# Kernel optimization log

Hardware: AMD Instinct MI355X
Metric: run time of the kernel (lower is better)

Reference implementation:

```python
import jax, jax.numpy as jnp
import numpy as np

N, IN_DIM, OUT_DIM, H = 4096, 128, 128, 4
HEAD_DIM = OUT_DIM // H
NEG_SLOPE = 0.2


def setup_inputs() -> dict:
    key = jax.random.key(0)
    k1, k2, k3, k4, k5 = jax.random.split(key, 5)
    x = jax.random.normal(k1, (N, IN_DIM), dtype=jnp.float32)
    adj = jax.random.randint(k2, (N, N), 0, 2, dtype=jnp.int32)
    # nn.Linear(in_dim, out_dim, bias=False): weight is [out_dim, in_dim]
    W = jax.random.normal(k3, (OUT_DIM, IN_DIM), dtype=jnp.float32) * (1.0 / np.sqrt(IN_DIM))
    attn_src = jax.random.normal(k4, (1, H, HEAD_DIM), dtype=jnp.float32) * 0.1
    attn_dst = jax.random.normal(k5, (1, H, HEAD_DIM), dtype=jnp.float32) * 0.1
    return {"x": x, "adj": adj, "W": W, "attn_src": attn_src, "attn_dst": attn_dst}


def reference(x, adj, W, attn_src, attn_dst):
    n = x.shape[0]
    h = (x @ W.T).reshape(n, H, HEAD_DIM)            # [N, H, D]
    e_src = jnp.sum(h * attn_src, axis=-1)           # [N, H]
    e_dst = jnp.sum(h * attn_dst, axis=-1)           # [N, H]
    e = e_src[:, None, :] + e_dst[None, :, :]        # [N, N, H]
    e = jax.nn.leaky_relu(e, negative_slope=NEG_SLOPE)
    e = jnp.where((adj == 0)[:, :, None], -jnp.inf, e)
    alpha = jax.nn.softmax(e, axis=1)                # softmax over neighbors j
    # dropout omitted (eval mode)
    out = jnp.einsum('ijh,jhd->ihd', alpha, h)       # [N, H, D]
    return out.reshape(n, -1)
```

## Files before the change

### kernel.cpp

```cpp
#include <hip/hip_runtime.h>
#include <hip/hip_bf16.h>

#define NN 4096
#define SJ 8
#define JCH (NN / SJ)
#define JSTEP 64
#define NSTEPS (JCH / JSTEP)
#define ROWS 16
#define LOG2E 1.44269504f

typedef __attribute__((ext_vector_type(4))) float f32x4;
typedef __attribute__((ext_vector_type(4))) int i32x4;
typedef __attribute__((ext_vector_type(4))) unsigned int u32x4;
typedef __attribute__((ext_vector_type(8))) short short8;

__device__ __forceinline__ unsigned pk2(float a, float b) {
    float2 t; t.x = a; t.y = b;
    __hip_bfloat162 h = __float22bfloat162_rn(t);
    unsigned r;
    __builtin_memcpy(&r, &h, 4);
    return r;
}

__device__ __forceinline__ short8 load8_bf(const float* __restrict__ p) {
    f32x4 a = *(const f32x4*)p;
    f32x4 b = *(const f32x4*)(p + 4);
    u32x4 v = {pk2(a[0], a[1]), pk2(a[2], a[3]), pk2(b[0], b[1]), pk2(b[2], b[3])};
    return __builtin_bit_cast(short8, v);
}

__global__ __launch_bounds__(256) void k1_proj(
        const float* __restrict__ x, const float* __restrict__ W,
        const float* __restrict__ asrc, const float* __restrict__ adst,
        unsigned short* __restrict__ hT, float* __restrict__ Rt,
        unsigned* __restrict__ BDt) {
    __shared__ unsigned short ttile[4][32][16];
    const int ibase = blockIdx.x * 16;
    const int w = threadIdx.x >> 6;
    const int lane = threadIdx.x & 63;
    const int grp = lane >> 4, li = lane & 15;

    const float* xrow = x + (ibase + li) * 128;
    const float* w0 = W + (w * 32 + li) * 128;
    const float* w1 = W + (w * 32 + 16 + li) * 128;

    f32x4 c0 = {0.f, 0.f, 0.f, 0.f}, c1 = {0.f, 0.f, 0.f, 0.f};
#pragma unroll
    for (int ko = 0; ko < 128; ko += 32) {
        const int kk = ko + grp * 8;
        short8 a = load8_bf(xrow + kk);
        short8 b0 = load8_bf(w0 + kk);
        short8 b1 = load8_bf(w1 + kk);
        c0 = __builtin_amdgcn_mfma_f32_16x16x32_bf16(a, b0, c0, 0, 0, 0);
        c1 = __builtin_amdgcn_mfma_f32_16x16x32_bf16(a, b1, c1, 0, 0, 0);
    }
    const float as0 = asrc[w * 32 + li], as1 = asrc[w * 32 + 16 + li];
    const float ad0 = adst[w * 32 + li], ad1 = adst[w * 32 + 16 + li];
    float pes[4], ped[4];
#pragma unroll
    for (int r = 0; r < 4; ++r) {
        pes[r] = c0[r] * as0 + c1[r] * as1;
        ped[r] = c0[r] * ad0 + c1[r] * ad1;
    }
#pragma unroll
    for (int m = 1; m < 16; m <<= 1) {
#pragma unroll
        for (int r = 0; r < 4; ++r) {
            pes[r] += __shfl_xor(pes[r], m);
            ped[r] += __shfl_xor(ped[r], m);
        }
    }
    if (li == 0) {
#pragma unroll
        for (int r = 0; r < 4; ++r) {
            const int row = ibase + grp * 4 + r;
            Rt[w * NN + row] = __builtin_amdgcn_exp2f(-0.8f * LOG2E * pes[r]);
            const float Bv = __builtin_amdgcn_exp2f(LOG2E * ped[r]);
            const float Dv = __builtin_amdgcn_exp2f(0.2f * LOG2E * ped[r]);
            BDt[w * NN + row] = pk2(Bv, Dv);
        }
    }
    unsigned short* tw = &ttile[w][0][0];
    {
        uint2 v0; v0.x = pk2(c0[0], c0[1]); v0.y = pk2(c0[2], c0[3]);
        uint2 v1; v1.x = pk2(c1[0], c1[1]); v1.y = pk2(c1[2], c1[3]);
        *(uint2*)&tw[li * 16 + grp * 4] = v0;
        *(uint2*)&tw[(li + 16) * 16 + grp * 4] = v1;
    }
    __syncthreads();
    const int d = lane >> 1, half = lane & 1;
    u32x4 v = *(const u32x4*)&ttile[w][d][half * 8];
    *(u32x4*)(hT + (size_t)(w * 32 + d) * NN + ibase + half * 8) = v;
}

struct SR {
    short8 t00, t01, t10, t11;
    u32x4 b0a, b0b, b1a, b1b;
};

__device__ __forceinline__ short8 buildQ(float R, const u32x4 ba, const u32x4 bb,
                                         const i32x4 q0, const i32x4 q1) {
    float p[8];
#pragma unroll
    for (int e = 0; e < 4; ++e) {
        const unsigned v = ba[e];
        const float B = __builtin_bit_cast(float, v << 16);
        const float D = __builtin_bit_cast(float, v & 0xFFFF0000u);
        const float m = fmaxf(B, R * D);
        p[e] = __builtin_bit_cast(float, __builtin_bit_cast(unsigned, m) & (0u - (unsigned)q0[e]));
    }
#pragma unroll
    for (int e = 0; e < 4; ++e) {
        const unsigned v = bb[e];
        const float B = __builtin_bit_cast(float, v << 16);
        const float D = __builtin_bit_cast(float, v & 0xFFFF0000u);
        const float m = fmaxf(B, R * D);
        p[4 + e] = __builtin_bit_cast(float, __builtin_bit_cast(unsigned, m) & (0u - (unsigned)q1[e]));
    }
    u32x4 u = {pk2(p[0], p[1]), pk2(p[2], p[3]), pk2(p[4], p[5]), pk2(p[6], p[7])};
    return __builtin_bit_cast(short8, u);
}

__global__ __launch_bounds__(256, 4) void k3_main(
        const int* __restrict__ adj, const unsigned short* __restrict__ hT,
        const float* __restrict__ Rt, const unsigned* __restrict__ BDt,
        float* __restrict__ numer, float* __restrict__ denom) {
    __shared__ unsigned int adjbuf[3][ROWS * 64];

    const int ibase = blockIdx.x * ROWS;
    const int jstart = blockIdx.y * JCH;
    const int head = threadIdx.x >> 6;
    const int lane = threadIdx.x & 63;
    const int grp = lane >> 4, li = lane & 15;

    const float Rv = Rt[head * NN + ibase + li];
    const unsigned short* h0 = hT + (size_t)(head * 32 + li) * NN + jstart;
    const unsigned short* h1 = hT + (size_t)(head * 32 + 16 + li) * NN + jstart;
    const unsigned* bd = BDt + head * NN + jstart;
    const unsigned int* adju = (const unsigned int*)adj;

    const int srow = head * 4 + grp;
    const unsigned int* gsrc = adju + (size_t)(ibase + srow) * NN + jstart + (li ^ srow) * 4;

    f32x4 c0 = {0.f,0.f,0.f,0.f}, c1 = {0.f,0.f,0.f,0.f}, dn = {0.f,0.f,0.f,0.f};
    short8 bones;
#pragma unroll
    for (int e = 0; e < 8; ++e) bones[e] = (short)0x3F80;

    auto stage = [&](int slot, int toff) {
        __builtin_amdgcn_global_load_lds(gsrc + toff, &adjbuf[slot][head * 4 * 64], 16, 0, 0);
    };
    auto loadR = [&](int toff) {
        SR r;
        r.t00 = *(const short8*)(h0 + toff + grp * 8);
        r.t01 = *(const short8*)(h0 + toff + 32 + grp * 8);
        r.t10 = *(const short8*)(h1 + toff + grp * 8);
        r.t11 = *(const short8*)(h1 + toff + 32 + grp * 8);
        r.b0a = *(const u32x4*)(bd + toff + grp * 8);
        r.b0b = *(const u32x4*)(bd + toff + grp * 8 + 4);
        r.b1a = *(const u32x4*)(bd + toff + 32 + grp * 8);
        r.b1b = *(const u32x4*)(bd + toff + 32 + grp * 8 + 4);
        return r;
    };
    auto compute = [&](const unsigned int* buf, const SR& S) {
#pragma unroll
        for (int ks = 0; ks < 2; ++ks) {
            const short8 tA = ks ? S.t01 : S.t00;
            const short8 tB = ks ? S.t11 : S.t10;
            const u32x4 ba = ks ? S.b1a : S.b0a;
            const u32x4 bb = ks ? S.b1b : S.b0b;
            const int cb = ks * 8 + grp * 2;
            const i32x4 q0 = *(const i32x4*)&buf[li * 64 + (cb ^ li) * 4];
            const i32x4 q1 = *(const i32x4*)&buf[li * 64 + ((cb + 1) ^ li) * 4];
            const short8 A = buildQ(Rv, ba, bb, q0, q1);
            c0 = __builtin_amdgcn_mfma_f32_16x16x32_bf16(A, tA, c0, 0, 0, 0);
            c1 = __builtin_amdgcn_mfma_f32_16x16x32_bf16(A, tB, c1, 0, 0, 0);
            dn = __builtin_amdgcn_mfma_f32_16x16x32_bf16(A, bones, dn, 0, 0, 0);
        }
    };

    SR S[2];
    stage(0, 0);
    S[0] = loadR(0);
    stage(1, JSTEP);
    asm volatile("s_waitcnt vmcnt(1)" ::: "memory");
    __builtin_amdgcn_s_barrier();
    __builtin_amdgcn_sched_barrier(0);

#pragma unroll
    for (int t = 0; t < NSTEPS; ++t) {
        if (t + 1 < NSTEPS) S[(t + 1) & 1] = loadR((t + 1) * JSTEP);
        if (t + 2 < NSTEPS) stage((t + 2) % 3, (t + 2) * JSTEP);

        compute(&adjbuf[t % 3][0], S[t & 1]);

        if (t + 2 < NSTEPS) {
            asm volatile("s_waitcnt vmcnt(1)" ::: "memory");
        } else if (t + 1 < NSTEPS) {
            asm volatile("s_waitcnt vmcnt(0)" ::: "memory");
        }
        if (t + 1 < NSTEPS) {
            __builtin_amdgcn_s_barrier();
            __builtin_amdgcn_sched_barrier(0);
        }
    }

    const int r0 = ibase + grp * 4;
    float* nb = numer + head * 32 + li;
#pragma unroll
    for (int r = 0; r < 4; ++r) {
        atomicAdd(nb + (size_t)(r0 + r) * 128, c0[r]);
        atomicAdd(nb + (size_t)(r0 + r) * 128 + 16, c1[r]);
    }
    if (li == 0) {
#pragma unroll
        for (int r = 0; r < 4; ++r)
            atomicAdd(denom + (r0 + r) * 4 + head, dn[r]);
    }
}

__global__ __launch_bounds__(256) void k4_fin(const float* __restrict__ numer,
                                              const float* __restrict__ denom,
                                              float* __restrict__ out) {
    const int idx = blockIdx.x * 256 + threadIdx.x;
    const int node = idx >> 7;
    const int headc = (idx & 127) >> 5;
    out[idx] = numer[idx] / denom[node * 4 + headc];
}

extern "C" void kernel_launch(void* const* d_in, const int* in_sizes, int n_in,
                              void* d_out, int out_size, void* d_ws, size_t ws_size,
                              hipStream_t stream) {
    const float* x = (const float*)d_in[0];
    const int* adj = (const int*)d_in[1];
    const float* W = (const float*)d_in[2];
    const float* asrc = (const float*)d_in[3];
    const float* adst = (const float*)d_in[4];
    float* out = (float*)d_out;

    char* ws = (char*)d_ws;
    float* numer = (float*)ws;
    float* denom = (float*)(ws + (size_t)2097152);
    float* Rt = (float*)(ws + (size_t)2097152 + 65536);
    unsigned* BDt = (unsigned*)(ws + (size_t)2097152 + 131072);
    unsigned short* hT = (unsigned short*)(ws + (size_t)2097152 + 196608);

    (void)hipMemsetAsync(numer, 0, 2097152 + 65536, stream);
    k1_proj<<<256, 256, 0, stream>>>(x, W, asrc, adst, hT, Rt, BDt);
    k3_main<<<dim3(NN / ROWS, SJ), 256, 0, stream>>>(adj, hT, Rt, BDt, numer, denom);
    k4_fin<<<2048, 256, 0, stream>>>(numer, denom, out);
}
```

Measured before the change: 66.73 us.

## Switch attention weights to packed fp16 math and load adjacency directly into registers

```diff
diff --git a/kernel.cpp b/kernel.cpp
--- a/kernel.cpp
+++ b/kernel.cpp
@@ -6,13 +6,13 @@
 #define JCH (NN / SJ)
 #define JSTEP 64
 #define NSTEPS (JCH / JSTEP)
-#define ROWS 16
 #define LOG2E 1.44269504f
 
 typedef __attribute__((ext_vector_type(4))) float f32x4;
 typedef __attribute__((ext_vector_type(4))) int i32x4;
 typedef __attribute__((ext_vector_type(4))) unsigned int u32x4;
 typedef __attribute__((ext_vector_type(8))) short short8;
+typedef __attribute__((ext_vector_type(8))) _Float16 f16x8;
 
 __device__ __forceinline__ unsigned pk2(float a, float b) {
     float2 t; t.x = a; t.y = b;
@@ -21,6 +21,11 @@
     __builtin_memcpy(&r, &h, 4);
     return r;
 }
+__device__ __forceinline__ unsigned pkh(float a, float b) {
+    unsigned short lo = __builtin_bit_cast(unsigned short, (_Float16)a);
+    unsigned short hi = __builtin_bit_cast(unsigned short, (_Float16)b);
+    return (unsigned)lo | ((unsigned)hi << 16);
+}
 
 __device__ __forceinline__ short8 load8_bf(const float* __restrict__ p) {
     f32x4 a = *(const f32x4*)p;
@@ -32,8 +37,8 @@
 __global__ __launch_bounds__(256) void k1_proj(
         const float* __restrict__ x, const float* __restrict__ W,
         const float* __restrict__ asrc, const float* __restrict__ adst,
-        unsigned short* __restrict__ hT, float* __restrict__ Rt,
-        unsigned* __restrict__ BDt) {
+        unsigned short* __restrict__ hf, float* __restrict__ Rt,
+        unsigned short* __restrict__ Bf, unsigned short* __restrict__ Df) {
     __shared__ unsigned short ttile[4][32][16];
     const int ibase = blockIdx.x * 16;
     const int w = threadIdx.x >> 6;
@@ -77,133 +82,140 @@
             Rt[w * NN + row] = __builtin_amdgcn_exp2f(-0.8f * LOG2E * pes[r]);
             const float Bv = __builtin_amdgcn_exp2f(LOG2E * ped[r]);
             const float Dv = __builtin_amdgcn_exp2f(0.2f * LOG2E * ped[r]);
-            BDt[w * NN + row] = pk2(Bv, Dv);
+            Bf[w * NN + row] = __builtin_bit_cast(unsigned short, (_Float16)Bv);
+            Df[w * NN + row] = __builtin_bit_cast(unsigned short, (_Float16)Dv);
         }
     }
     unsigned short* tw = &ttile[w][0][0];
     {
-        uint2 v0; v0.x = pk2(c0[0], c0[1]); v0.y = pk2(c0[2], c0[3]);
-        uint2 v1; v1.x = pk2(c1[0], c1[1]); v1.y = pk2(c1[2], c1[3]);
+        uint2 v0; v0.x = pkh(c0[0], c0[1]); v0.y = pkh(c0[2], c0[3]);
+        uint2 v1; v1.x = pkh(c1[0], c1[1]); v1.y = pkh(c1[2], c1[3]);
         *(uint2*)&tw[li * 16 + grp * 4] = v0;
         *(uint2*)&tw[(li + 16) * 16 + grp * 4] = v1;
     }
     __syncthreads();
     const int d = lane >> 1, half = lane & 1;
     u32x4 v = *(const u32x4*)&ttile[w][d][half * 8];
-    *(u32x4*)(hT + (size_t)(w * 32 + d) * NN + ibase + half * 8) = v;
-}
-
-struct SR {
-    short8 t00, t01, t10, t11;
-    u32x4 b0a, b0b, b1a, b1b;
-};
-
-__device__ __forceinline__ short8 buildQ(float R, const u32x4 ba, const u32x4 bb,
-                                         const i32x4 q0, const i32x4 q1) {
-    float p[8];
-#pragma unroll
-    for (int e = 0; e < 4; ++e) {
-        const unsigned v = ba[e];
-        const float B = __builtin_bit_cast(float, v << 16);
-        const float D = __builtin_bit_cast(float, v & 0xFFFF0000u);
-        const float m = fmaxf(B, R * D);
-        p[e] = __builtin_bit_cast(float, __builtin_bit_cast(unsigned, m) & (0u - (unsigned)q0[e]));
-    }
-#pragma unroll
-    for (int e = 0; e < 4; ++e) {
-        const unsigned v = bb[e];
-        const float B = __builtin_bit_cast(float, v << 16);
-        const float D = __builtin_bit_cast(float, v & 0xFFFF0000u);
-        const float m = fmaxf(B, R * D);
-        p[4 + e] = __builtin_bit_cast(float, __builtin_bit_cast(unsigned, m) & (0u - (unsigned)q1[e]));
-    }
-    u32x4 u = {pk2(p[0], p[1]), pk2(p[2], p[3]), pk2(p[4], p[5]), pk2(p[6], p[7])};
-    return __builtin_bit_cast(short8, u);
-}
-
-__global__ __launch_bounds__(256, 4) void k3_main(
-        const int* __restrict__ adj, const unsigned short* __restrict__ hT,
-        const float* __restrict__ Rt, const unsigned* __restrict__ BDt,
+    *(u32x4*)(hf + (size_t)(w * 32 + d) * NN + ibase + half * 8) = v;
+}
+
+template<int OFF>
+__device__ __forceinline__ u32x4 gld(const void* p) {
+    u32x4 d;
+    asm volatile("global_load_dwordx4 %0, %1, off offset:%c2"
+                 : "=&v"(d) : "v"(p), "n"(OFF));
+    return d;
+}
+
+struct SLOT { u32x4 q00, q01, q10, q11, t00, t01, t10, t11, b0, b1, d0, d1; };
+
+#define LOADSET(S, TT) do {                                                    \
+    (S).q00 = gld<(TT)*256 +   0>(aB);  (S).q01 = gld<(TT)*256 +  16>(aB);     \
+    (S).q10 = gld<(TT)*256 + 128>(aB);  (S).q11 = gld<(TT)*256 + 144>(aB);     \
+    (S).t00 = gld<(TT)*128 +   0>(h0b); (S).t01 = gld<(TT)*128 +  64>(h0b);    \
+    (S).t10 = gld<(TT)*128 +   0>(h1b); (S).t11 = gld<(TT)*128 +  64>(h1b);    \
+    (S).b0  = gld<(TT)*128 +   0>(Bb);  (S).b1  = gld<(TT)*128 +  64>(Bb);     \
+    (S).d0  = gld<(TT)*128 +   0>(Db);  (S).d1  = gld<(TT)*128 +  64>(Db);     \
+} while (0)
+
+#define LAUNDER(S) asm volatile("" : "+v"((S).q00), "+v"((S).q01),             \
+    "+v"((S).q10), "+v"((S).q11), "+v"((S).t00), "+v"((S).t01),                \
+    "+v"((S).t10), "+v"((S).t11), "+v"((S).b0), "+v"((S).b1),                  \
+    "+v"((S).d0), "+v"((S).d1))
+
+__device__ __forceinline__ unsigned pmm(unsigned Rp, unsigned B2, unsigned D2,
+                                        unsigned a0, unsigned a1) {
+    unsigned rd, mx;
+    asm("v_pk_mul_f16 %0, %1, %2" : "=v"(rd) : "v"(Rp), "v"(D2));
+    asm("v_pk_max_f16 %0, %1, %2" : "=v"(mx) : "v"(B2), "v"(rd));
+    const unsigned mask = __builtin_amdgcn_perm(0u - a1, 0u - a0, 0x05040100u);
+    return mx & mask;
+}
+
+__device__ __forceinline__ f16x8 buildA(unsigned Rp, const u32x4 B, const u32x4 D,
+                                        const u32x4 q0, const u32x4 q1) {
+    u32x4 w;
+    w[0] = pmm(Rp, B[0], D[0], q0[0], q0[1]);
+    w[1] = pmm(Rp, B[1], D[1], q0[2], q0[3]);
+    w[2] = pmm(Rp, B[2], D[2], q1[0], q1[1]);
+    w[3] = pmm(Rp, B[3], D[3], q1[2], q1[3]);
+    return __builtin_bit_cast(f16x8, w);
+}
+
+__global__ __launch_bounds__(256) void k3_main(
+        const int* __restrict__ adj, const unsigned short* __restrict__ hf,
+        const float* __restrict__ Rt, const unsigned short* __restrict__ Bf,
+        const unsigned short* __restrict__ Df,
         float* __restrict__ numer, float* __restrict__ denom) {
-    __shared__ unsigned int adjbuf[3][ROWS * 64];
-
-    const int ibase = blockIdx.x * ROWS;
+    const int ibase = blockIdx.x * 16;
     const int jstart = blockIdx.y * JCH;
     const int head = threadIdx.x >> 6;
     const int lane = threadIdx.x & 63;
     const int grp = lane >> 4, li = lane & 15;
 
     const float Rv = Rt[head * NN + ibase + li];
-    const unsigned short* h0 = hT + (size_t)(head * 32 + li) * NN + jstart;
-    const unsigned short* h1 = hT + (size_t)(head * 32 + 16 + li) * NN + jstart;
-    const unsigned* bd = BDt + head * NN + jstart;
-    const unsigned int* adju = (const unsigned int*)adj;
-
-    const int srow = head * 4 + grp;
-    const unsigned int* gsrc = adju + (size_t)(ibase + srow) * NN + jstart + (li ^ srow) * 4;
+    const unsigned short ru = __builtin_bit_cast(unsigned short, (_Float16)Rv);
+    const unsigned Rp = (unsigned)ru | ((unsigned)ru << 16);
+
+    const int* aB = adj + (size_t)(ibase + li) * NN + jstart + grp * 8;
+    const unsigned short* h0b = hf + (size_t)(head * 32 + li) * NN + jstart + grp * 8;
+    const unsigned short* h1b = h0b + (size_t)16 * NN;
+    const unsigned short* Bb = Bf + head * NN + jstart + grp * 8;
+    const unsigned short* Db = Df + head * NN + jstart + grp * 8;
 
     f32x4 c0 = {0.f,0.f,0.f,0.f}, c1 = {0.f,0.f,0.f,0.f}, dn = {0.f,0.f,0.f,0.f};
-    short8 bones;
-#pragma unroll
-    for (int e = 0; e < 8; ++e) bones[e] = (short)0x3F80;
-
-    auto stage = [&](int slot, int toff) {
-        __builtin_amdgcn_global_load_lds(gsrc + toff, &adjbuf[slot][head * 4 * 64], 16, 0, 0);
-    };
-    auto loadR = [&](int toff) {
-        SR r;
-        r.t00 = *(const short8*)(h0 + toff + grp * 8);
-        r.t01 = *(const short8*)(h0 + toff + 32 + grp * 8);
-        r.t10 = *(const short8*)(h1 + toff + grp * 8);
-        r.t11 = *(const short8*)(h1 + toff + 32 + grp * 8);
-        r.b0a = *(const u32x4*)(bd + toff + grp * 8);
-        r.b0b = *(const u32x4*)(bd + toff + grp * 8 + 4);
-        r.b1a = *(const u32x4*)(bd + toff + 32 + grp * 8);
-        r.b1b = *(const u32x4*)(bd + toff + 32 + grp * 8 + 4);
-        return r;
-    };
-    auto compute = [&](const unsigned int* buf, const SR& S) {
-#pragma unroll
-        for (int ks = 0; ks < 2; ++ks) {
-            const short8 tA = ks ? S.t01 : S.t00;
-            const short8 tB = ks ? S.t11 : S.t10;
-            const u32x4 ba = ks ? S.b1a : S.b0a;
-            const u32x4 bb = ks ? S.b1b : S.b0b;
-            const int cb = ks * 8 + grp * 2;
-            const i32x4 q0 = *(const i32x4*)&buf[li * 64 + (cb ^ li) * 4];
-            const i32x4 q1 = *(const i32x4*)&buf[li * 64 + ((cb + 1) ^ li) * 4];
-            const short8 A = buildQ(Rv, ba, bb, q0, q1);
-            c0 = __builtin_amdgcn_mfma_f32_16x16x32_bf16(A, tA, c0, 0, 0, 0);
-            c1 = __builtin_amdgcn_mfma_f32_16x16x32_bf16(A, tB, c1, 0, 0, 0);
-            dn = __builtin_amdgcn_mfma_f32_16x16x32_bf16(A, bones, dn, 0, 0, 0);
-        }
-    };
-
-    SR S[2];
-    stage(0, 0);
-    S[0] = loadR(0);
-    stage(1, JSTEP);
-    asm volatile("s_waitcnt vmcnt(1)" ::: "memory");
-    __builtin_amdgcn_s_barrier();
+    u32x4 onesw = {0x3C003C00u, 0x3C003C00u, 0x3C003C00u, 0x3C003C00u};
+    const f16x8 ones = __builtin_bit_cast(f16x8, onesw);
+
+    SLOT s0, s1, s2;
+
+#define COMPUTE(S) do {                                                        \
+    _Pragma("unroll")                                                          \
+    for (int ks = 0; ks < 2; ++ks) {                                           \
+        const u32x4 ba = ks ? (S).b1 : (S).b0;                                 \
+        const u32x4 da = ks ? (S).d1 : (S).d0;                                 \
+        const u32x4 qa = ks ? (S).q10 : (S).q00;                               \
+        const u32x4 qb = ks ? (S).q11 : (S).q01;                               \
+        const f16x8 tA = __builtin_bit_cast(f16x8, ks ? (S).t01 : (S).t00);    \
+        const f16x8 tB = __builtin_bit_cast(f16x8, ks ? (S).t11 : (S).t10);    \
+        const f16x8 A = buildA(Rp, ba, da, qa, qb);                            \
+        c0 = __builtin_amdgcn_mfma_f32_16x16x32_f16(A, tA, c0, 0, 0, 0);       \
+        c1 = __builtin_amdgcn_mfma_f32_16x16x32_f16(A, tB, c1, 0, 0, 0);       \
+        dn = __builtin_amdgcn_mfma_f32_16x16x32_f16(A, ones, dn, 0, 0, 0);     \
+    }                                                                          \
+} while (0)
+
+#define STEP(T, CUR, NXT, FAR) do {                                            \
+    if ((T) + 2 < NSTEPS) { LOADSET(FAR, (T) + 2); }                           \
+    __builtin_amdgcn_sched_barrier(0);                                         \
+    COMPUTE(CUR);                                                              \
+    if ((T) + 1 < NSTEPS) {                                                    \
+        if ((T) + 2 < NSTEPS) {                                                \
+            asm volatile("s_waitcnt vmcnt(12)" ::: "memory");                  \
+        } else {                                                               \
+            asm volatile("s_waitcnt vmcnt(0)" ::: "memory");                   \
+        }                                                                      \
+        LAUNDER(NXT);                                                          \
+        __builtin_amdgcn_sched_barrier(0);                                     \
+    }                                                                          \
+} while (0)
+
+    LOADSET(s0, 0);
     __builtin_amdgcn_sched_barrier(0);
-
-#pragma unroll
-    for (int t = 0; t < NSTEPS; ++t) {
-        if (t + 1 < NSTEPS) S[(t + 1) & 1] = loadR((t + 1) * JSTEP);
-        if (t + 2 < NSTEPS) stage((t + 2) % 3, (t + 2) * JSTEP);
-
-        compute(&adjbuf[t % 3][0], S[t & 1]);
-
-        if (t + 2 < NSTEPS) {
-            asm volatile("s_waitcnt vmcnt(1)" ::: "memory");
-        } else if (t + 1 < NSTEPS) {
-            asm volatile("s_waitcnt vmcnt(0)" ::: "memory");
-        }
-        if (t + 1 < NSTEPS) {
-            __builtin_amdgcn_s_barrier();
-            __builtin_amdgcn_sched_barrier(0);
-        }
-    }
+    LOADSET(s1, 1);
+    __builtin_amdgcn_sched_barrier(0);
+    asm volatile("s_waitcnt vmcnt(12)" ::: "memory");
+    LAUNDER(s0);
+    __builtin_amdgcn_sched_barrier(0);
+
+    STEP(0, s0, s1, s2);
+    STEP(1, s1, s2, s0);
+    STEP(2, s2, s0, s1);
+    STEP(3, s0, s1, s2);
+    STEP(4, s1, s2, s0);
+    STEP(5, s2, s0, s1);
+    STEP(6, s0, s1, s2);
+    STEP(7, s1, s2, s0);
 
     const int r0 = ibase + grp * 4;
     float* nb = numer + head * 32 + li;
@@ -217,6 +229,8 @@
         for (int r = 0; r < 4; ++r)
             atomicAdd(denom + (r0 + r) * 4 + head, dn[r]);
     }
+#undef STEP
+#undef COMPUTE
 }
 
 __global__ __launch_bounds__(256) void k4_fin(const float* __restrict__ numer,
@@ -241,12 +255,13 @@
     char* ws = (char*)d_ws;
     float* numer = (float*)ws;
     float* denom = (float*)(ws + (size_t)2097152);
-    float* Rt = (float*)(ws + (size_t)2097152 + 65536);
-    unsigned* BDt = (unsigned*)(ws + (size_t)2097152 + 131072);
-    unsigned short* hT = (unsigned short*)(ws + (size_t)2097152 + 196608);
+    float* Rt = (float*)(ws + (size_t)2162688);
+    unsigned short* Bf = (unsigned short*)(ws + (size_t)2228224);
+    unsigned short* Df = (unsigned short*)(ws + (size_t)2260992);
+    unsigned short* hf = (unsigned short*)(ws + (size_t)2293760);
 
     (void)hipMemsetAsync(numer, 0, 2097152 + 65536, stream);
-    k1_proj<<<256, 256, 0, stream>>>(x, W, asrc, adst, hT, Rt, BDt);
-    k3_main<<<dim3(NN / ROWS, SJ), 256, 0, stream>>>(adj, hT, Rt, BDt, numer, denom);
+    k1_proj<<<256, 256, 0, stream>>>(x, W, asrc, adst, hf, Rt, Bf, Df);
+    k3_main<<<dim3(256, SJ), 256, 0, stream>>>(adj, hf, Rt, Bf, Df, numer, denom);
     k4_fin<<<2048, 256, 0, stream>>>(numer, denom, out);
 }
```

After: 91.13 us. +36.6%, slower.

## Pack adjacency into bitmask in pre-pass and restructure main kernel per head

Applied to the files above, without the earlier changes.

```diff
diff --git a/kernel.cpp b/kernel.cpp
--- a/kernel.cpp
+++ b/kernel.cpp
@@ -6,7 +6,6 @@
 #define JCH (NN / SJ)
 #define JSTEP 64
 #define NSTEPS (JCH / JSTEP)
-#define ROWS 16
 #define LOG2E 1.44269504f
 
 typedef __attribute__((ext_vector_type(4))) float f32x4;
@@ -27,6 +26,26 @@
     f32x4 b = *(const f32x4*)(p + 4);
     u32x4 v = {pk2(a[0], a[1]), pk2(a[2], a[3]), pk2(b[0], b[1]), pk2(b[2], b[3])};
     return __builtin_bit_cast(short8, v);
+}
+
+__global__ __launch_bounds__(256) void k0_mask(const int* __restrict__ adj,
+                                               unsigned long long* __restrict__ maskv) {
+    const int wave = threadIdx.x >> 6;
+    const int lane = threadIdx.x & 63;
+    const int row = blockIdx.x * 4 + wave;
+    const int* src = adj + (size_t)row * NN + lane * 4;
+#pragma unroll 4
+    for (int c = 0; c < 16; ++c) {
+        const i32x4 v = *(const i32x4*)(src + c * 256);
+        const unsigned long long w0 = __ballot(v[0] != 0);
+        const unsigned long long w1 = __ballot(v[1] != 0);
+        const unsigned long long w2 = __ballot(v[2] != 0);
+        const unsigned long long w3 = __ballot(v[3] != 0);
+        if (lane == 0) {
+            unsigned long long* d = maskv + (size_t)row * 64 + c * 4;
+            d[0] = w0; d[1] = w1; d[2] = w2; d[3] = w3;
+        }
+    }
 }
 
 __global__ __launch_bounds__(256) void k1_proj(
@@ -93,117 +112,127 @@
     *(u32x4*)(hT + (size_t)(w * 32 + d) * NN + ibase + half * 8) = v;
 }
 
-struct SR {
-    short8 t00, t01, t10, t11;
-    u32x4 b0a, b0b, b1a, b1b;
-};
-
-__device__ __forceinline__ short8 buildQ(float R, const u32x4 ba, const u32x4 bb,
-                                         const i32x4 q0, const i32x4 q1) {
+template<int OFF>
+__device__ __forceinline__ u32x4 gld(const void* p) {
+    u32x4 d;
+    asm volatile("global_load_dwordx4 %0, %1, off offset:%c2"
+                 : "=&v"(d) : "v"(p), "n"(OFF));
+    return d;
+}
+
+struct SR { u32x4 h0k0, h0k1, h1k0, h1k1, bd00, bd01, bd10, bd11, ma, mb; };
+
+#define LOADSET(S, T) do {                                                       \
+    (S).h0k0 = gld<(T)*128      >(h0b); (S).h0k1 = gld<(T)*128 +  64>(h0b);      \
+    (S).h1k0 = gld<(T)*128      >(h1b); (S).h1k1 = gld<(T)*128 +  64>(h1b);      \
+    (S).bd00 = gld<(T)*256      >(bd);  (S).bd01 = gld<(T)*256 +  16>(bd);       \
+    (S).bd10 = gld<(T)*256 + 128>(bd);  (S).bd11 = gld<(T)*256 + 144>(bd);       \
+    (S).ma   = gld<((T)>>2)*32    >(pm0); (S).mb  = gld<((T)>>2)*32 + 16>(pm0);  \
+} while (0)
+
+#define LAUNDER(s) asm volatile("" : "+v"((s).h0k0), "+v"((s).h0k1),             \
+    "+v"((s).h1k0), "+v"((s).h1k1), "+v"((s).bd00), "+v"((s).bd01),              \
+    "+v"((s).bd10), "+v"((s).bd11), "+v"((s).ma), "+v"((s).mb))
+
+__device__ __forceinline__ short8 buildQb(float R, const u32x4 ba, const u32x4 bb,
+                                          const u32x4 ma, const u32x4 mb,
+                                          const int L0, const int shb) {
+    const bool hi = (L0 >= 32);
+    const int l0 = L0 & 31;
+    unsigned wsel[4];
+    wsel[0] = hi ? ma[1] : ma[0];
+    wsel[1] = hi ? ma[3] : ma[2];
+    wsel[2] = hi ? mb[1] : mb[0];
+    wsel[3] = hi ? mb[3] : mb[2];
     float p[8];
 #pragma unroll
-    for (int e = 0; e < 4; ++e) {
-        const unsigned v = ba[e];
+    for (int e = 0; e < 8; ++e) {
+        const unsigned v = (e < 4) ? ba[e] : bb[e - 4];
         const float B = __builtin_bit_cast(float, v << 16);
         const float D = __builtin_bit_cast(float, v & 0xFFFF0000u);
         const float m = fmaxf(B, R * D);
-        p[e] = __builtin_bit_cast(float, __builtin_bit_cast(unsigned, m) & (0u - (unsigned)q0[e]));
-    }
-#pragma unroll
-    for (int e = 0; e < 4; ++e) {
-        const unsigned v = bb[e];
-        const float B = __builtin_bit_cast(float, v << 16);
-        const float D = __builtin_bit_cast(float, v & 0xFFFF0000u);
-        const float m = fmaxf(B, R * D);
-        p[4 + e] = __builtin_bit_cast(float, __builtin_bit_cast(unsigned, m) & (0u - (unsigned)q1[e]));
+        const unsigned bit = (wsel[e & 3] >> (l0 + shb + (e >> 2))) & 1u;
+        p[e] = __builtin_bit_cast(float, __builtin_bit_cast(unsigned, m) & (0u - bit));
     }
     u32x4 u = {pk2(p[0], p[1]), pk2(p[2], p[3]), pk2(p[4], p[5]), pk2(p[6], p[7])};
     return __builtin_bit_cast(short8, u);
 }
 
-__global__ __launch_bounds__(256, 4) void k3_main(
-        const int* __restrict__ adj, const unsigned short* __restrict__ hT,
+__global__ __launch_bounds__(64) void k3_main(
+        const unsigned long long* __restrict__ maskv,
+        const unsigned short* __restrict__ hT,
         const float* __restrict__ Rt, const unsigned* __restrict__ BDt,
         float* __restrict__ numer, float* __restrict__ denom) {
-    __shared__ unsigned int adjbuf[3][ROWS * 64];
-
-    const int ibase = blockIdx.x * ROWS;
-    const int jstart = blockIdx.y * JCH;
-    const int head = threadIdx.x >> 6;
-    const int lane = threadIdx.x & 63;
+    const int head = blockIdx.x;
+    const int ibase = blockIdx.y * 16;
+    const int jstart = blockIdx.z * JCH;
+    const int lane = threadIdx.x;
     const int grp = lane >> 4, li = lane & 15;
-
-    const float Rv = Rt[head * NN + ibase + li];
-    const unsigned short* h0 = hT + (size_t)(head * 32 + li) * NN + jstart;
-    const unsigned short* h1 = hT + (size_t)(head * 32 + 16 + li) * NN + jstart;
-    const unsigned* bd = BDt + head * NN + jstart;
-    const unsigned int* adju = (const unsigned int*)adj;
-
-    const int srow = head * 4 + grp;
-    const unsigned int* gsrc = adju + (size_t)(ibase + srow) * NN + jstart + (li ^ srow) * 4;
+    const int shb = grp * 2;
+
+    const float R0 = Rt[head * NN + ibase + li];
+    const unsigned short* h0b = hT + (size_t)(head * 32 + li) * NN + jstart + grp * 8;
+    const unsigned short* h1b = h0b + (size_t)16 * NN;
+    const unsigned* bd = BDt + head * NN + jstart + grp * 8;
+    const unsigned long long* pm0 = maskv + (size_t)(ibase + li) * 64 + (jstart >> 8) * 4;
 
     f32x4 c0 = {0.f,0.f,0.f,0.f}, c1 = {0.f,0.f,0.f,0.f}, dn = {0.f,0.f,0.f,0.f};
     short8 bones;
 #pragma unroll
     for (int e = 0; e < 8; ++e) bones[e] = (short)0x3F80;
 
-    auto stage = [&](int slot, int toff) {
-        __builtin_amdgcn_global_load_lds(gsrc + toff, &adjbuf[slot][head * 4 * 64], 16, 0, 0);
-    };
-    auto loadR = [&](int toff) {
-        SR r;
-        r.t00 = *(const short8*)(h0 + toff + grp * 8);
-        r.t01 = *(const short8*)(h0 + toff + 32 + grp * 8);
-        r.t10 = *(const short8*)(h1 + toff + grp * 8);
-        r.t11 = *(const short8*)(h1 + toff + 32 + grp * 8);
-        r.b0a = *(const u32x4*)(bd + toff + grp * 8);
-        r.b0b = *(const u32x4*)(bd + toff + grp * 8 + 4);
-        r.b1a = *(const u32x4*)(bd + toff + 32 + grp * 8);
-        r.b1b = *(const u32x4*)(bd + toff + 32 + grp * 8 + 4);
-        return r;
-    };
-    auto compute = [&](const unsigned int* buf, const SR& S) {
-#pragma unroll
-        for (int ks = 0; ks < 2; ++ks) {
-            const short8 tA = ks ? S.t01 : S.t00;
-            const short8 tB = ks ? S.t11 : S.t10;
-            const u32x4 ba = ks ? S.b1a : S.b0a;
-            const u32x4 bb = ks ? S.b1b : S.b0b;
-            const int cb = ks * 8 + grp * 2;
-            const i32x4 q0 = *(const i32x4*)&buf[li * 64 + (cb ^ li) * 4];
-            const i32x4 q1 = *(const i32x4*)&buf[li * 64 + ((cb + 1) ^ li) * 4];
-            const short8 A = buildQ(Rv, ba, bb, q0, q1);
-            c0 = __builtin_amdgcn_mfma_f32_16x16x32_bf16(A, tA, c0, 0, 0, 0);
-            c1 = __builtin_amdgcn_mfma_f32_16x16x32_bf16(A, tB, c1, 0, 0, 0);
-            dn = __builtin_amdgcn_mfma_f32_16x16x32_bf16(A, bones, dn, 0, 0, 0);
-        }
-    };
-
-    SR S[2];
-    stage(0, 0);
-    S[0] = loadR(0);
-    stage(1, JSTEP);
-    asm volatile("s_waitcnt vmcnt(1)" ::: "memory");
-    __builtin_amdgcn_s_barrier();
+    SR s0, s1, s2;
+
+#define COMPUTE(S, T) do {                                                       \
+    _Pragma("unroll")                                                            \
+    for (int ks = 0; ks < 2; ++ks) {                                             \
+        const u32x4 ba = ks ? (S).bd10 : (S).bd00;                               \
+        const u32x4 bb = ks ? (S).bd11 : (S).bd01;                               \
+        const short8 tA = __builtin_bit_cast(short8, ks ? (S).h0k1 : (S).h0k0);  \
+        const short8 tB = __builtin_bit_cast(short8, ks ? (S).h1k1 : (S).h1k0);  \
+        const short8 A = buildQb(R0, ba, bb, (S).ma, (S).mb,                     \
+                                 ((T) & 3) * 16 + ks * 8, shb);                  \
+        c0 = __builtin_amdgcn_mfma_f32_16x16x32_bf16(A, tA, c0, 0, 0, 0);        \
+        c1 = __builtin_amdgcn_mfma_f32_16x16x32_bf16(A, tB, c1, 0, 0, 0);        \
+        dn = __builtin_amdgcn_mfma_f32_16x16x32_bf16(A, bones, dn, 0, 0, 0);     \
+    }                                                                            \
+} while (0)
+
+#define STEP(T, CUR, NXT, FAR) do {                                              \
+    if ((T) + 2 < NSTEPS) {                                                      \
+        LOADSET(FAR, (T) + 2);                                                   \
+        __builtin_amdgcn_sched_barrier(0);                                       \
+    }                                                                            \
+    COMPUTE(CUR, T);                                                             \
+    if ((T) + 1 < NSTEPS) {                                                      \
+        if ((T) + 2 < NSTEPS) {                                                  \
+            asm volatile("s_waitcnt vmcnt(10)" ::: "memory");                    \
+        } else {                                                                 \
+            asm volatile("s_waitcnt vmcnt(0)" ::: "memory");                     \
+        }                                                                        \
+        LAUNDER(NXT);                                                            \
+        __builtin_amdgcn_sched_barrier(0);                                       \
+    }                                                                            \
+} while (0)
+
+    LOADSET(s0, 0);
     __builtin_amdgcn_sched_barrier(0);
-
-#pragma unroll
-    for (int t = 0; t < NSTEPS; ++t) {
-        if (t + 1 < NSTEPS) S[(t + 1) & 1] = loadR((t + 1) * JSTEP);
-        if (t + 2 < NSTEPS) stage((t + 2) % 3, (t + 2) * JSTEP);
-
-        compute(&adjbuf[t % 3][0], S[t & 1]);
-
-        if (t + 2 < NSTEPS) {
-            asm volatile("s_waitcnt vmcnt(1)" ::: "memory");
-        } else if (t + 1 < NSTEPS) {
-            asm volatile("s_waitcnt vmcnt(0)" ::: "memory");
-        }
-        if (t + 1 < NSTEPS) {
-            __builtin_amdgcn_s_barrier();
-            __builtin_amdgcn_sched_barrier(0);
-        }
-    }
+    LOADSET(s1, 1);
+    __builtin_amdgcn_sched_barrier(0);
+    asm volatile("s_waitcnt vmcnt(10)" ::: "memory");
+    LAUNDER(s0);
+    __builtin_amdgcn_sched_barrier(0);
+
+    STEP(0, s0, s1, s2);
+    STEP(1, s1, s2, s0);
+    STEP(2, s2, s0, s1);
+    STEP(3, s0, s1, s2);
+    STEP(4, s1, s2, s0);
+    STEP(5, s2, s0, s1);
+    STEP(6, s0, s1, s2);
+    STEP(7, s1, s2, s0);
+#undef STEP
+#undef COMPUTE
 
     const int r0 = ibase + grp * 4;
     float* nb = numer + head * 32 + li;
@@ -244,9 +273,11 @@
     float* Rt = (float*)(ws + (size_t)2097152 + 65536);
     unsigned* BDt = (unsigned*)(ws + (size_t)2097152 + 131072);
     unsigned short* hT = (unsigned short*)(ws + (size_t)2097152 + 196608);
+    unsigned long long* maskv = (unsigned long long*)(ws + (size_t)2097152 + 196608 + 1048576);
 
     (void)hipMemsetAsync(numer, 0, 2097152 + 65536, stream);
+    k0_mask<<<1024, 256, 0, stream>>>(adj, maskv);
     k1_proj<<<256, 256, 0, stream>>>(x, W, asrc, adst, hT, Rt, BDt);
-    k3_main<<<dim3(NN / ROWS, SJ), 256, 0, stream>>>(adj, hT, Rt, BDt, numer, denom);
+    k3_main<<<dim3(4, 256, SJ), 64, 0, stream>>>(maskv, hT, Rt, BDt, numer, denom);
     k4_fin<<<2048, 256, 0, stream>>>(numer, denom, out);
 }
```

New measurement: 87.26 us. 30.8% more time.
